# Performance work log

Measured on AMD Instinct MI355X. Metric: run time of the kernel, lower is better.

The kernel has to match this reference:

```python
import jax, jax.numpy as jnp
import numpy as np

N, NV, E0, HID, L, H = 32768, 64, 524288, 128, 4, 8
D = HID // H  # 16
SCALE = 1.0 / float(np.sqrt(D))


def _segment_softmax(logits, seg, num_segments):
    # numerically stable softmax grouped by destination node (leading axis = edges)
    m = jax.ops.segment_max(logits, seg, num_segments=num_segments)
    m = jnp.where(jnp.isfinite(m), m, 0.0)  # guard empty segments
    e = jnp.exp(logits - m[seg])
    s = jax.ops.segment_sum(e, seg, num_segments=num_segments)
    return e / (s[seg] + 1e-16)


def _forward(ei0, ei1, x_op, x_v, Wk, bk, Wq, bq, Wv, bv, Wa, ba, skip,
             a_rel, m_rel, p_rel, jk_w_in, jk_b_in, jk_w_out, jk_b_out,
             nm_w0, nm_b0, nm_w1, nm_b1, nm_w2, nm_b2, nm_w3, nm_b3,
             nm_w4, nm_b4, nm_w5, nm_b5, nm_w6, nm_b6,
             gm_w0, gm_b0, gm_w1, gm_b1):
    s0, d0 = ei0[0], ei0[1]
    s1, d1 = ei1[0], ei1[1]
    nm_ws = (nm_w0, nm_w1, nm_w2, nm_w3, nm_w4, nm_w5, nm_w6)
    nm_bs = (nm_b0, nm_b1, nm_b2, nm_b3, nm_b4, nm_b5, nm_b6)
    proj = lambda x, W, b: (x @ W.T + b).reshape(x.shape[0], H, D)
    outs_v = []
    for l in range(L):  # HGTConv layers (node types: 0='op', 1='virtual_op')
        k_op = proj(x_op, Wk[l, 0], bk[l, 0])
        q_op = proj(x_op, Wq[l, 0], bq[l, 0])
        v_op = proj(x_op, Wv[l, 0], bv[l, 0])
        q_v = proj(x_v, Wq[l, 1], bq[l, 1])  # virtual nodes only receive messages
        # relation 0: op -> op
        k0 = jnp.einsum('nhd,hde->nhe', k_op, a_rel[l, 0])
        v0 = jnp.einsum('nhd,hde->nhe', v_op, m_rel[l, 0])
        lg0 = jnp.sum(q_op[d0] * k0[s0], -1) * p_rel[l, 0] * SCALE  # [E0, H]
        al0 = _segment_softmax(lg0, d0, N)
        agg_op = jax.ops.segment_sum(al0[..., None] * v0[s0], d0, num_segments=N).reshape(N, HID)
        # relation 1: op -> virtual_op
        k1 = jnp.einsum('nhd,hde->nhe', k_op, a_rel[l, 1])
        v1 = jnp.einsum('nhd,hde->nhe', v_op, m_rel[l, 1])
        lg1 = jnp.sum(q_v[d1] * k1[s1], -1) * p_rel[l, 1] * SCALE  # [E1, H]
        al1 = _segment_softmax(lg1, d1, NV)
        agg_v = jax.ops.segment_sum(al1[..., None] * v1[s1], d1, num_segments=NV).reshape(NV, HID)
        # target-specific output projection + sigmoid-gated skip (in == out channels)
        o_op = jax.nn.gelu(agg_op, approximate=False) @ Wa[l, 0].T + ba[l, 0]
        g = jax.nn.sigmoid(skip[l, 0])
        x_op = g * o_op + (1.0 - g) * x_op
        o_v = jax.nn.gelu(agg_v, approximate=False) @ Wa[l, 1].T + ba[l, 1]
        g = jax.nn.sigmoid(skip[l, 1])
        x_v = g * o_v + (1.0 - g) * x_v
        outs_v.append(x_v)
    # JK via MultiheadAttention: seq = L layers, batch = NV virtual nodes
    xs = jnp.stack(outs_v)  # [L, NV, HID]
    qkv = xs @ jk_w_in.T + jk_b_in
    q, k, v = jnp.split(qkv, 3, axis=-1)
    q = q.reshape(L, NV, H, D)
    k = k.reshape(L, NV, H, D)
    v = v.reshape(L, NV, H, D)
    attn = jax.nn.softmax(jnp.einsum('qbhd,kbhd->bhqk', q, k) * SCALE, axis=-1)
    o = jnp.einsum('bhqk,kbhd->qbhd', attn, v).reshape(L, NV, HID)
    o = o @ jk_w_out.T + jk_b_out
    h = o.sum(0)  # [NV, HID]; batch_size == NV (1 virtual node per graph)
    for w_, b_ in zip(nm_ws[:-1], nm_bs[:-1]):  # node MLP (GELU hidden layers)
        h = jax.nn.gelu(h @ w_.T + b_, approximate=False)
    h = h @ nm_ws[-1].T + nm_bs[-1]  # [NV, 1]
    h = jax.nn.gelu(h @ gm_w0.T + gm_b0, approximate=False)  # graph MLP
    h = h @ gm_w1.T + gm_b1  # [NV, 1]
    return h[:, 0]  # squeeze(1)


def setup_inputs() -> dict:
    key = jax.random.key(0)
    ks = iter(jax.random.split(key, 64))
    nk = lambda: next(ks)
    w = lambda shape, s: jax.random.normal(nk(), shape, jnp.float32) * s
    inp = {}
    inp['x_op'] = jax.random.normal(nk(), (N, HID), jnp.float32)
    inp['x_v'] = jax.random.normal(nk(), (NV, HID), jnp.float32)
    src0 = jax.random.randint(nk(), (E0,), 0, N, jnp.int32)
    dst0 = jax.random.randint(nk(), (E0,), 0, N, jnp.int32)
    inp['ei0'] = jnp.stack([src0, dst0])
    batch_op = jax.random.randint(nk(), (N,), 0, NV, jnp.int32)  # graph id of each op node
    inp['ei1'] = jnp.stack([jnp.arange(N, dtype=jnp.int32), batch_op])
    for nm in ('Wk', 'Wq', 'Wv', 'Wa'):
        inp[nm] = w((L, 2, HID, HID), 0.1)
    for nm in ('bk', 'bq', 'bv', 'ba'):
        inp[nm] = jnp.zeros((L, 2, HID), jnp.float32)
    inp['skip'] = jnp.ones((L, 2), jnp.float32)
    inp['a_rel'] = w((L, 2, H, D, D), 0.25)
    inp['m_rel'] = w((L, 2, H, D, D), 0.25)
    inp['p_rel'] = jnp.ones((L, 2, H), jnp.float32)
    inp['jk_w_in'] = w((3 * HID, HID), 0.1)
    inp['jk_b_in'] = jnp.zeros((3 * HID,), jnp.float32)
    inp['jk_w_out'] = w((HID, HID), 0.1)
    inp['jk_b_out'] = jnp.zeros((HID,), jnp.float32)
    dims = [128, 64, 32, 16, 8, 4, 2, 1]  # _get_mlp_layer_dims(128, 1) + final out
    for i in range(7):
        inp[f'nm_w{i}'] = w((dims[i + 1], dims[i]), (2.0 / dims[i]) ** 0.5)
        inp[f'nm_b{i}'] = jnp.zeros((dims[i + 1],), jnp.float32)
    inp['gm_w0'] = w((2, 1), 1.0)
    inp['gm_b0'] = jnp.zeros((2,), jnp.float32)
    inp['gm_w1'] = w((1, 2), 0.7)
    inp['gm_b1'] = jnp.zeros((1,), jnp.float32)
    return inp


def reference(x_op, x_v, ei0, ei1, Wk, bk, Wq, bq, Wv, bv, Wa, ba, skip,
              a_rel, m_rel, p_rel, jk_w_in, jk_b_in, jk_w_out, jk_b_out,
              nm_w0, nm_b0, nm_w1, nm_b1, nm_w2, nm_b2, nm_w3, nm_b3,
              nm_w4, nm_b4, nm_w5, nm_b5, nm_w6, nm_b6,
              gm_w0, gm_b0, gm_w1, gm_b1):
    return _forward(ei0, ei1, x_op, x_v, Wk, bk, Wq, bq, Wv, bv, Wa, ba, skip,
                    a_rel, m_rel, p_rel, jk_w_in, jk_b_in, jk_w_out, jk_b_out,
                    nm_w0, nm_b0, nm_w1, nm_b1, nm_w2, nm_b2, nm_w3, nm_b3,
                    nm_w4, nm_b4, nm_w5, nm_b5, nm_w6, nm_b6,
                    gm_w0, gm_b0, gm_w1, gm_b1)
```

## Files before the change

kernel.cpp:

```cpp
#include <hip/hip_runtime.h>

#define NN   32768
#define NV   64
#define E0E  524288
#define HID  128
#define NL   4
#define NH   8
#define DH   16
#define SCALE 0.25f
#define LDA  136
#define CAP0 64
#define CAP1 1024

typedef __attribute__((ext_vector_type(8))) short short8;
typedef __attribute__((ext_vector_type(4))) float f32x4;

__device__ __forceinline__ float gelu_f(float x) {
  return 0.5f * x * (1.0f + erff(x * 0.7071067811865475f));
}
__device__ __forceinline__ float sigmoid_f(float x) {
  return 1.0f / (1.0f + __expf(-x));
}
__device__ __forceinline__ unsigned short f2bf(float x) {
  unsigned u = __float_as_uint(x);
  return (unsigned short)((u + 0x7FFFu + ((u >> 16) & 1u)) >> 16);
}
__device__ __forceinline__ float bf2f(unsigned short h) {
  return __uint_as_float(((unsigned)h) << 16);
}
__device__ __forceinline__ unsigned short f2h(float x) {
  union { _Float16 h; unsigned short u; } cv;
  cv.h = (_Float16)x;
  return cv.u;
}
__device__ __forceinline__ float h2f(unsigned short u) {
  union { _Float16 h; unsigned short u; } cv;
  cv.u = u;
  return (float)cv.h;
}
__device__ __forceinline__ float f16lo(unsigned u) { return h2f((unsigned short)(u & 0xffffu)); }
__device__ __forceinline__ float f16hi(unsigned u) { return h2f((unsigned short)(u >> 16)); }

union SMu {
  struct { unsigned short Ah[64][LDA]; unsigned short Al[64][LDA]; } a;
  struct { float xr[HID]; float xn[HID]; } v;
};

__device__ __forceinline__ void stage_A(unsigned short Ah[][LDA], unsigned short Al[][LDA],
                                        int t, const float* __restrict__ A, int m0, int gelu) {
  #pragma unroll
  for (int i = 0; i < 8; ++i) {
    int idx = t + 256 * i;
    int m = idx >> 5, c4 = (idx & 31) * 4;
    float4 v = *(const float4*)(A + (size_t)(m0 + m) * HID + c4);
    if (gelu) { v.x = gelu_f(v.x); v.y = gelu_f(v.y); v.z = gelu_f(v.z); v.w = gelu_f(v.w); }
    unsigned short h0 = f2bf(v.x), h1 = f2bf(v.y), h2 = f2bf(v.z), h3 = f2bf(v.w);
    *(ushort4*)&Ah[m][c4] = make_ushort4(h0, h1, h2, h3);
    *(ushort4*)&Al[m][c4] = make_ushort4(f2bf(v.x - bf2f(h0)), f2bf(v.y - bf2f(h1)),
                                         f2bf(v.z - bf2f(h2)), f2bf(v.w - bf2f(h3)));
  }
}

__device__ __forceinline__ void mfma_pass(const unsigned short Ah[][LDA],
    const unsigned short Al[][LDA], int t, const unsigned short* __restrict__ Wf,
    f32x4 acc[2][4]) {
  const int w = t >> 6, lane = t & 63, c16 = lane & 15, quad = lane >> 4;
  #pragma unroll
  for (int ks = 0; ks < 4; ++ks) {
    short8 ah[4], al[4];
    #pragma unroll
    for (int s = 0; s < 4; ++s) {
      ah[s] = *(const short8*)&Ah[16 * s + c16][ks * 32 + quad * 8];
      al[s] = *(const short8*)&Al[16 * s + c16][ks * 32 + quad * 8];
    }
    #pragma unroll
    for (int j = 0; j < 2; ++j) {
      const unsigned short* bp = Wf + (size_t)(((2 * w + j) * 4 + ks) * 64 + lane) * 8;
      short8 bh = *(const short8*)bp;
      short8 bl = *(const short8*)(bp + 16384);
      #pragma unroll
      for (int s = 0; s < 4; ++s) {
        acc[j][s] = __builtin_amdgcn_mfma_f32_16x16x32_bf16(ah[s], bh, acc[j][s], 0, 0, 0);
        acc[j][s] = __builtin_amdgcn_mfma_f32_16x16x32_bf16(ah[s], bl, acc[j][s], 0, 0, 0);
        acc[j][s] = __builtin_amdgcn_mfma_f32_16x16x32_bf16(al[s], bh, acc[j][s], 0, 0, 0);
      }
    }
  }
}

__device__ __forceinline__ void proj_q(const unsigned short Ah[][LDA],
    const unsigned short Al[][LDA], int t, int m0,
    const unsigned short* __restrict__ WqF, const float* __restrict__ bq0,
    float* __restrict__ Pq) {
  const int w = t >> 6, c16 = t & 15, quad = (t & 63) >> 4;
  f32x4 acc[2][4] = {};
  mfma_pass(Ah, Al, t, WqF, acc);
  #pragma unroll
  for (int j = 0; j < 2; ++j) {
    const int col = (2 * w + j) * 16 + c16;
    const float bb = bq0[col];
    #pragma unroll
    for (int s = 0; s < 4; ++s)
      #pragma unroll
      for (int r = 0; r < 4; ++r) {
        int m = m0 + 16 * s + quad * 4 + r;
        Pq[(size_t)m * HID + col] = acc[j][s][r] + bb;
      }
  }
}

__device__ __forceinline__ void proj_kv(const unsigned short Ah[][LDA],
    const unsigned short Al[][LDA], int t, int m0,
    const unsigned short* __restrict__ WfK, const float* __restrict__ bK,
    const float* __restrict__ bV, unsigned int* __restrict__ dst) {
  const int w = t >> 6, c16 = t & 15, quad = (t & 63) >> 4;
  unsigned kp[2][4][2];
  {
    f32x4 accK[2][4] = {};
    mfma_pass(Ah, Al, t, WfK, accK);
    #pragma unroll
    for (int j = 0; j < 2; ++j) {
      const float bbk = bK[(2 * w + j) * 16 + c16];
      #pragma unroll
      for (int s = 0; s < 4; ++s)
        #pragma unroll
        for (int rr = 0; rr < 2; ++rr)
          kp[j][s][rr] = (unsigned)f2h(accK[j][s][2 * rr] + bbk)
                       | ((unsigned)f2h(accK[j][s][2 * rr + 1] + bbk) << 16);
    }
  }
  f32x4 accV[2][4] = {};
  mfma_pass(Ah, Al, t, WfK + 32768, accV);
  #pragma unroll
  for (int j = 0; j < 2; ++j) {
    const int col = (2 * w + j) * 16 + c16;
    const float bbv = bV[col];
    #pragma unroll
    for (int s = 0; s < 4; ++s)
      #pragma unroll
      for (int r = 0; r < 4; ++r) {
        int m = m0 + 16 * s + quad * 4 + r;
        unsigned pk = (kp[j][s][r >> 1] >> ((r & 1) * 16)) & 0xffffu;
        unsigned pv = (unsigned)f2h(accV[j][s][r] + bbv);
        dst[(size_t)m * HID + col] = pk | (pv << 16);
      }
  }
}

__global__ __launch_bounds__(256) void k_setup(
    const float* __restrict__ Wk, const float* __restrict__ Wv,
    const float* __restrict__ bk, const float* __restrict__ bv,
    const float* __restrict__ a_rel, const float* __restrict__ m_rel,
    const float* __restrict__ p_rel,
    float* __restrict__ CW, float* __restrict__ CB) {
  int blk = blockIdx.x, t = threadIdx.x;
  int l = blk >> 2, mat = blk & 3;
  int rel = mat >> 1;
  int isK = ((mat & 1) == 0);
  const float* W  = (isK ? Wk : Wv) + (size_t)(l * 2) * HID * HID;
  const float* bb = (isK ? bk : bv) + (l * 2) * HID;
  const float* R  = (isK ? a_rel : m_rel) + (size_t)((l * 2 + rel) * NH) * DH * DH;
  float* cw = CW + (size_t)blk * HID * HID;
  float* cb = CB + blk * HID;
  for (int o = t; o < HID * HID; o += 256) {
    int j = o >> 7, c = o & 127;
    int h = j >> 4, e = j & 15;
    float sc = isK ? (p_rel[(l * 2 + rel) * NH + h] * SCALE) : 1.0f;
    float s = 0.f;
    #pragma unroll
    for (int d = 0; d < DH; ++d)
      s += W[(size_t)(h * DH + d) * HID + c] * R[h * 256 + d * 16 + e];
    cw[(size_t)j * HID + c] = s * sc;
  }
  if (t < HID) {
    int j = t, h = j >> 4, e = j & 15;
    float sc = isK ? (p_rel[(l * 2 + rel) * NH + h] * SCALE) : 1.0f;
    float s = 0.f;
    #pragma unroll
    for (int d = 0; d < DH; ++d) s += bb[h * DH + d] * R[h * 256 + d * 16 + e];
    cb[j] = s * sc;
  }
}

__global__ __launch_bounds__(256) void k_frag(const float* __restrict__ CW,
                                              const float* __restrict__ Wq,
                                              const float* __restrict__ Wa,
                                              unsigned short* __restrict__ FW) {
  int m = blockIdx.x, t = threadIdx.x;
  const float* src = (m < 16) ? (CW + (size_t)m * HID * HID)
                   : (m < 20) ? (Wq + (size_t)((m - 16) * 2) * HID * HID)
                              : (Wa + (size_t)((m - 20) * 2) * HID * HID);
  unsigned short* hi = FW + (size_t)m * 32768;
  unsigned short* lo = hi + 16384;
  for (int idx = t; idx < 16384; idx += 256) {
    int j = idx & 7, lane = (idx >> 3) & 63, ks = (idx >> 9) & 3, nt = idx >> 11;
    int n = nt * 16 + (lane & 15);
    int k = ks * 32 + (lane >> 4) * 8 + j;
    float x = src[(size_t)n * HID + k];
    unsigned short h = f2bf(x);
    hi[idx] = h;
    lo[idx] = f2bf(x - bf2f(h));
  }
}

struct PreArgs {
  const int *src0, *dst0, *src1, *dst1;
  int *cnt0, *cnt1, *colB0, *colB1;
  const float* x_op; const unsigned short* FW; const float *bq, *CB;
  float* Pq; unsigned int *Pkv0, *Pkv1;
  const float *x_v, *Wq1, *bq1; float* qv;
};

__launch_bounds__(256)
__global__ void k_pre(PreArgs a) {
  __shared__ SMu sm;
  int bx = blockIdx.x, t = threadIdx.x;
  if (bx < E0E / 1024) {
    int base = bx * 1024 + t;
    #pragma unroll
    for (int i = 0; i < 4; ++i) {
      int e = base + i * 256;
      int d = a.dst0[e];
      int pos = atomicAdd(&a.cnt0[d], 1);
      if (pos < CAP0) a.colB0[((size_t)d << 6) + pos] = a.src0[e];
    }
    return;
  }
  bx -= E0E / 1024;
  if (bx < NN / 1024) {
    int base = bx * 1024 + t;
    #pragma unroll
    for (int i = 0; i < 4; ++i) {
      int e = base + i * 256;
      int d = a.dst1[e];
      int pos = atomicAdd(&a.cnt1[d], 1);
      if (pos < CAP1) a.colB1[((size_t)d << 10) + pos] = a.src1[e];
    }
    return;
  }
  bx -= NN / 1024;
  if (bx < 3 * (NN / 64)) {
    int y = bx >> 9, tile = bx & 511;
    int m0 = tile * 64;
    stage_A(sm.a.Ah, sm.a.Al, t, a.x_op, m0, 0);
    __syncthreads();
    if (y == 0)      proj_q (sm.a.Ah, sm.a.Al, t, m0, a.FW + (size_t)16 * 32768, a.bq, a.Pq);
    else if (y == 1) proj_kv(sm.a.Ah, sm.a.Al, t, m0, a.FW, a.CB, a.CB + HID, a.Pkv0);
    else             proj_kv(sm.a.Ah, sm.a.Al, t, m0, a.FW + (size_t)2 * 32768,
                             a.CB + 2 * HID, a.CB + 3 * HID, a.Pkv1);
    return;
  }
  bx -= 3 * (NN / 64);
  if (t < HID) sm.v.xr[t] = a.x_v[bx * HID + t];
  __syncthreads();
  if (t < HID) {
    float s = a.bq1[t];
    const float4* wr = (const float4*)(a.Wq1 + (size_t)t * HID);
    const float4* xx = (const float4*)sm.v.xr;
    #pragma unroll 8
    for (int c = 0; c < HID / 4; ++c) {
      float4 w4 = wr[c], x4 = xx[c];
      s += x4.x * w4.x + x4.y * w4.y + x4.z * w4.z + x4.w * w4.w;
    }
    a.qv[bx * HID + t] = s;
  }
}

__launch_bounds__(256)
__global__ void k_edges(const float* __restrict__ Pq, const unsigned int* __restrict__ Pkv0,
                        const unsigned int* __restrict__ Pkv1,
                        const int* __restrict__ cnt0, const int* __restrict__ colB0,
                        float* __restrict__ agg, const float* __restrict__ qv,
                        const int* __restrict__ cnt1, const int* __restrict__ colB1,
                        float* __restrict__ part, int e0blocks) {
  int lane = threadIdx.x & 63;
  if (blockIdx.x < e0blocks) {
    int n = blockIdx.x * 4 + (threadIdx.x >> 6);
    float2 q = *(const float2*)(Pq + (size_t)n * HID + 2 * lane);
    int cnt = cnt0[n]; if (cnt > CAP0) cnt = CAP0;
    int e = n << 6, e1 = (n << 6) + cnt;
    float acc0 = 0.f, acc1 = 0.f, wsum = 0.f;
    for (; e + 8 <= e1; e += 8) {
      const uint2* r[8];
      #pragma unroll
      for (int u = 0; u < 8; ++u)
        r[u] = (const uint2*)(Pkv0 + ((size_t)colB0[e + u] << 7) + 2 * lane);
      uint2 kv[8];
      #pragma unroll
      for (int u = 0; u < 8; ++u) kv[u] = *r[u];
      float p[8];
      #pragma unroll
      for (int u = 0; u < 8; ++u)
        p[u] = q.x * f16lo(kv[u].x) + q.y * f16lo(kv[u].y);
      #pragma unroll
      for (int u = 0; u < 8; ++u) {
        p[u] += __shfl_xor(p[u], 1); p[u] += __shfl_xor(p[u], 2); p[u] += __shfl_xor(p[u], 4);
      }
      #pragma unroll
      for (int u = 0; u < 8; ++u) {
        float wg = __expf(p[u]);
        wsum += wg; acc0 += wg * f16hi(kv[u].x); acc1 += wg * f16hi(kv[u].y);
      }
    }
    for (; e < e1; ++e) {
      uint2 kv = *(const uint2*)(Pkv0 + ((size_t)colB0[e] << 7) + 2 * lane);
      float p = q.x * f16lo(kv.x) + q.y * f16lo(kv.y);
      p += __shfl_xor(p, 1); p += __shfl_xor(p, 2); p += __shfl_xor(p, 4);
      float wg = __expf(p);
      wsum += wg; acc0 += wg * f16hi(kv.x); acc1 += wg * f16hi(kv.y);
    }
    float inv = 1.0f / (wsum + 1e-16f);
    *(float2*)(agg + (size_t)n * HID + 2 * lane) = make_float2(acc0 * inv, acc1 * inv);
  } else {
    int b2 = blockIdx.x - e0blocks;
    int g = b2 >> 3, ch = b2 & 7;
    int w = threadIdx.x >> 6;
    int slot = ch * 4 + w;
    float2 q = *(const float2*)(qv + g * HID + 2 * lane);
    int tot = cnt1[g]; if (tot > CAP1) tot = CAP1;
    int base = g << 10;
    int len = (tot + 31) >> 5;
    int s0 = base + slot * len;
    int s1 = s0 + len; int lim = base + tot; if (s1 > lim) s1 = lim;
    float acc0 = 0.f, acc1 = 0.f, wsum = 0.f;
    int e = s0;
    for (; e + 4 <= s1; e += 4) {
      uint2 ka = *(const uint2*)(Pkv1 + ((size_t)colB1[e]     << 7) + 2 * lane);
      uint2 kb = *(const uint2*)(Pkv1 + ((size_t)colB1[e + 1] << 7) + 2 * lane);
      uint2 kc = *(const uint2*)(Pkv1 + ((size_t)colB1[e + 2] << 7) + 2 * lane);
      uint2 kd = *(const uint2*)(Pkv1 + ((size_t)colB1[e + 3] << 7) + 2 * lane);
      float pa = q.x * f16lo(ka.x) + q.y * f16lo(ka.y);
      float pb = q.x * f16lo(kb.x) + q.y * f16lo(kb.y);
      float pc = q.x * f16lo(kc.x) + q.y * f16lo(kc.y);
      float pd = q.x * f16lo(kd.x) + q.y * f16lo(kd.y);
      pa += __shfl_xor(pa, 1); pb += __shfl_xor(pb, 1); pc += __shfl_xor(pc, 1); pd += __shfl_xor(pd, 1);
      pa += __shfl_xor(pa, 2); pb += __shfl_xor(pb, 2); pc += __shfl_xor(pc, 2); pd += __shfl_xor(pd, 2);
      pa += __shfl_xor(pa, 4); pb += __shfl_xor(pb, 4); pc += __shfl_xor(pc, 4); pd += __shfl_xor(pd, 4);
      float wa = __expf(pa), wb = __expf(pb), wc = __expf(pc), wd = __expf(pd);
      wsum += (wa + wb) + (wc + wd);
      acc0 += wa * f16hi(ka.x) + wb * f16hi(kb.x) + wc * f16hi(kc.x) + wd * f16hi(kd.x);
      acc1 += wa * f16hi(ka.y) + wb * f16hi(kb.y) + wc * f16hi(kc.y) + wd * f16hi(kd.y);
    }
    for (; e < s1; ++e) {
      uint2 kv = *(const uint2*)(Pkv1 + ((size_t)colB1[e] << 7) + 2 * lane);
      float p = q.x * f16lo(kv.x) + q.y * f16lo(kv.y);
      p += __shfl_xor(p, 1); p += __shfl_xor(p, 2); p += __shfl_xor(p, 4);
      float ww = __expf(p);
      wsum += ww; acc0 += ww * f16hi(kv.x); acc1 += ww * f16hi(kv.y);
    }
    float* pp = part + (size_t)(g * 32 + slot) * 192;
    pp[lane] = acc0; pp[64 + lane] = acc1; pp[128 + lane] = wsum;
  }
}

struct PArgs {
  const float *agg; const unsigned short *WaF_l; const float *ba_l0, *skip_l0, *xold;
  float *xop;
  const float *part, *Wa_l1, *ba_l1, *skip_l1, *xvold;
  float *xv, *outsv_l, *qv;
  const float *Wq_n1, *bq_n1;
  int do_qv;
  const unsigned short *WqF_n, *CWF_n;
  const float *bq_n0, *CB_n;
  float *Pq; unsigned int *Pkv0, *Pkv1;
  int mode;
};

__device__ __forceinline__ void vtail(SMu& sm, int t, int v, const PArgs& f) {
  if (t < 64) {
    float a0 = 0.f, a1 = 0.f, ws2 = 0.f;
    for (int s = 0; s < 32; ++s) {
      const float* p = f.part + (size_t)(v * 32 + s) * 192;
      a0 += p[t]; a1 += p[64 + t]; ws2 += p[128 + t];
    }
    float inv = 1.0f / (ws2 + 1e-16f);
    sm.v.xr[2 * t]     = gelu_f(a0 * inv);
    sm.v.xr[2 * t + 1] = gelu_f(a1 * inv);
  }
  __syncthreads();
  if (t < HID) {
    float s = f.ba_l1[t];
    const float4* wr = (const float4*)(f.Wa_l1 + (size_t)t * HID);
    const float4* xx = (const float4*)sm.v.xr;
    #pragma unroll 8
    for (int c = 0; c < HID / 4; ++c) {
      float4 w4 = wr[c], x4 = xx[c];
      s += x4.x * w4.x + x4.y * w4.y + x4.z * w4.z + x4.w * w4.w;
    }
    float gg = sigmoid_f(*f.skip_l1);
    float nv2 = gg * s + (1.f - gg) * f.xvold[v * HID + t];
    f.xv[v * HID + t] = nv2;
    f.outsv_l[v * HID + t] = nv2;
    sm.v.xn[t] = nv2;
  }
  __syncthreads();
  if (f.do_qv && t < HID) {
    float s = f.bq_n1[t];
    const float4* wr = (const float4*)(f.Wq_n1 + (size_t)t * HID);
    const float4* xx = (const float4*)sm.v.xn;
    #pragma unroll 8
    for (int c = 0; c < HID / 4; ++c) {
      float4 w4 = wr[c], x4 = xx[c];
      s += x4.x * w4.x + x4.y * w4.y + x4.z * w4.z + x4.w * w4.w;
    }
    f.qv[v * HID + t] = s;
  }
}

__launch_bounds__(256)
__global__ void k_post(PArgs f) {
  __shared__ SMu sm;
  const int t = threadIdx.x;
  int bx = blockIdx.x;
  if (f.mode == 2) { vtail(sm, t, bx, f); return; }
  if (bx >= NN / 64) { vtail(sm, t, bx - NN / 64, f); return; }
  const int m0 = bx * 64;
  stage_A(sm.a.Ah, sm.a.Al, t, f.agg, m0, 1);
  __syncthreads();
  f32x4 acc[2][4] = {};
  mfma_pass(sm.a.Ah, sm.a.Al, t, f.WaF_l, acc);
  const int w = t >> 6, c16 = t & 15, quad = (t & 63) >> 4;
  float g = sigmoid_f(*f.skip_l0), gm1 = 1.0f - g;
  #pragma unroll
  for (int j = 0; j < 2; ++j) {
    const int col = (2 * w + j) * 16 + c16;
    const float bb = f.ba_l0[col];
    #pragma unroll
    for (int s = 0; s < 4; ++s)
      #pragma unroll
      for (int r = 0; r < 4; ++r) {
        int lm = 16 * s + quad * 4 + r;
        float v = acc[j][s][r] + bb;
        v = g * v + gm1 * f.xold[(size_t)(m0 + lm) * HID + col];
        acc[j][s][r] = v;
        if (f.mode == 0)
          f.xop[(size_t)(m0 + lm) * HID + col] = v;
      }
  }
  __syncthreads();
  #pragma unroll
  for (int j = 0; j < 2; ++j) {
    const int col = (2 * w + j) * 16 + c16;
    #pragma unroll
    for (int s = 0; s < 4; ++s)
      #pragma unroll
      for (int r = 0; r < 4; ++r) {
        int lm = 16 * s + quad * 4 + r;
        float v = acc[j][s][r];
        unsigned short h = f2bf(v);
        sm.a.Ah[lm][col] = h;
        sm.a.Al[lm][col] = f2bf(v - bf2f(h));
      }
  }
  __syncthreads();
  if (f.mode == 1) {
    proj_kv(sm.a.Ah, sm.a.Al, t, m0, f.CWF_n + (size_t)2 * 32768,
            f.CB_n + 2 * HID, f.CB_n + 3 * HID, f.Pkv1);
    return;
  }
  proj_q (sm.a.Ah, sm.a.Al, t, m0, f.WqF_n, f.bq_n0, f.Pq);
  proj_kv(sm.a.Ah, sm.a.Al, t, m0, f.CWF_n, f.CB_n, f.CB_n + HID, f.Pkv0);
  proj_kv(sm.a.Ah, sm.a.Al, t, m0, f.CWF_n + (size_t)2 * 32768,
          f.CB_n + 2 * HID, f.CB_n + 3 * HID, f.Pkv1);
}

struct TailW {
  const float *win, *bin, *wout, *bout;
  const float *nw0, *nb0, *nw1, *nb1, *nw2, *nb2, *nw3, *nb3, *nw4, *nb4, *nw5, *nb5, *nw6, *nb6;
  const float *gw0, *gb0, *gw1, *gb1;
};

__launch_bounds__(128)
__global__ void k_final(const float* __restrict__ outsv, TailW tw, float* __restrict__ outp) {
  __shared__ float xs[4][HID], qq[4][HID], kk[4][HID], vv[4][HID], oo[4][HID];
  __shared__ float att[NH][4][4];
  __shared__ float hb[HID], tb[64];
  int b = blockIdx.x, t = threadIdx.x;
  for (int l = 0; l < 4; ++l) xs[l][t] = outsv[(size_t)(l * NV + b) * HID + t];
  __syncthreads();
  for (int l = 0; l < 4; ++l) {
    float sq = tw.bin[t], sk = tw.bin[t + 128], sv = tw.bin[t + 256];
    const float* wq = tw.win + (size_t)t * HID;
    const float* wk = tw.win + (size_t)(t + 128) * HID;
    const float* wv = tw.win + (size_t)(t + 256) * HID;
    for (int c = 0; c < HID; ++c) {
      float x = xs[l][c];
      sq += x * wq[c]; sk += x * wk[c]; sv += x * wv[c];
    }
    qq[l][t] = sq; kk[l][t] = sk; vv[l][t] = sv;
  }
  __syncthreads();
  {
    int h = t >> 4, ql = (t >> 2) & 3, kl = t & 3;
    float s = 0.f;
    #pragma unroll
    for (int d = 0; d < DH; ++d) s += qq[ql][h * DH + d] * kk[kl][h * DH + d];
    att[h][ql][kl] = s * SCALE;
  }
  __syncthreads();
  if (t < 32) {
    int h = t >> 2, ql = t & 3;
    float m = att[h][ql][0];
    for (int k2 = 1; k2 < 4; ++k2) m = fmaxf(m, att[h][ql][k2]);
    float e[4], s = 0.f;
    for (int k2 = 0; k2 < 4; ++k2) { e[k2] = __expf(att[h][ql][k2] - m); s += e[k2]; }
    for (int k2 = 0; k2 < 4; ++k2) att[h][ql][k2] = e[k2] / s;
  }
  __syncthreads();
  {
    int h = t >> 4;
    #pragma unroll
    for (int ql = 0; ql < 4; ++ql) {
      float s = 0.f;
      #pragma unroll
      for (int kl = 0; kl < 4; ++kl) s += att[h][ql][kl] * vv[kl][t];
      oo[ql][t] = s;
    }
  }
  __syncthreads();
  {
    float s = 0.f;
    const float* wr = tw.wout + (size_t)t * HID;
    for (int l = 0; l < 4; ++l) {
      float ss = tw.bout[t];
      for (int c = 0; c < HID; ++c) ss += oo[l][c] * wr[c];
      s += ss;
    }
    hb[t] = s;
  }
  __syncthreads();
  if (t < 64) { float s = tw.nb0[t]; const float* wr = tw.nw0 + t * 128; for (int c = 0; c < 128; ++c) s += hb[c] * wr[c]; tb[t] = gelu_f(s); }
  __syncthreads();
  if (t < 32) { float s = tw.nb1[t]; const float* wr = tw.nw1 + t * 64;  for (int c = 0; c < 64;  ++c) s += tb[c] * wr[c]; hb[t] = gelu_f(s); }
  __syncthreads();
  if (t < 16) { float s = tw.nb2[t]; const float* wr = tw.nw2 + t * 32;  for (int c = 0; c < 32;  ++c) s += hb[c] * wr[c]; tb[t] = gelu_f(s); }
  __syncthreads();
  if (t < 8)  { float s = tw.nb3[t]; const float* wr = tw.nw3 + t * 16;  for (int c = 0; c < 16;  ++c) s += tb[c] * wr[c]; hb[t] = gelu_f(s); }
  __syncthreads();
  if (t < 4)  { float s = tw.nb4[t]; const float* wr = tw.nw4 + t * 8;   for (int c = 0; c < 8;   ++c) s += hb[c] * wr[c]; tb[t] = gelu_f(s); }
  __syncthreads();
  if (t < 2)  { float s = tw.nb5[t]; const float* wr = tw.nw5 + t * 4;   for (int c = 0; c < 4;   ++c) s += tb[c] * wr[c]; hb[t] = gelu_f(s); }
  __syncthreads();
  if (t == 0) {
    float s = hb[0] * tw.nw6[0] + hb[1] * tw.nw6[1] + tw.nb6[0];
    float g0 = gelu_f(s * tw.gw0[0] + tw.gb0[0]);
    float g1 = gelu_f(s * tw.gw0[1] + tw.gb0[1]);
    outp[b] = g0 * tw.gw1[0] + g1 * tw.gw1[1] + tw.gb1[0];
  }
}

extern "C" void kernel_launch(void* const* d_in, const int* in_sizes, int n_in,
                              void* d_out, int out_size, void* d_ws, size_t ws_size,
                              hipStream_t stream) {
  const float* x_op = (const float*)d_in[0];
  const float* x_v  = (const float*)d_in[1];
  const int*   ei0  = (const int*)d_in[2];
  const int*   ei1  = (const int*)d_in[3];
  const float* Wk   = (const float*)d_in[4];
  const float* Wq   = (const float*)d_in[5];
  const float* Wv   = (const float*)d_in[6];
  const float* Wa   = (const float*)d_in[7];
  const float* bk   = (const float*)d_in[8];
  const float* bq   = (const float*)d_in[9];
  const float* bv   = (const float*)d_in[10];
  const float* ba   = (const float*)d_in[11];
  const float* skip = (const float*)d_in[12];
  const float* a_rel = (const float*)d_in[13];
  const float* m_rel = (const float*)d_in[14];
  const float* p_rel = (const float*)d_in[15];
  (void)in_sizes; (void)n_in; (void)out_size; (void)ws_size;

  char* wsp = (char*)d_ws;
  size_t off = 0;
  auto alloc = [&](size_t bytes) -> void* {
    void* p = wsp + off;
    off += (bytes + 255) & ~(size_t)255;
    return p;
  };
  float* Pq    = (float*)alloc((size_t)NN * HID * 4);
  unsigned int* Pkv0 = (unsigned int*)alloc((size_t)NN * HID * 4);
  unsigned int* Pkv1 = (unsigned int*)alloc((size_t)NN * HID * 4);
  float* xop   = (float*)alloc((size_t)NN * HID * 4);
  float* agg   = (float*)alloc((size_t)NN * HID * 4);
  float* CW    = (float*)alloc((size_t)16 * HID * HID * 4);
  float* CB    = (float*)alloc((size_t)16 * HID * 4);
  unsigned short* FW = (unsigned short*)alloc((size_t)24 * 32768 * 2);
  float* xv    = (float*)alloc((size_t)NV * HID * 4);
  float* qv    = (float*)alloc((size_t)NV * HID * 4);
  float* outsv = (float*)alloc((size_t)NL * NV * HID * 4);
  float* part  = (float*)alloc((size_t)NV * 32 * 192 * 4);
  int* cnt0    = (int*)alloc((size_t)NN * 4);
  int* colB0   = (int*)alloc((size_t)NN * CAP0 * 4);
  int* cnt1    = (int*)alloc((size_t)NV * 4);
  int* colB1   = (int*)alloc((size_t)NV * CAP1 * 4);

  hipMemsetAsync(cnt0, 0, (size_t)NN * 4, stream);
  hipMemsetAsync(cnt1, 0, (size_t)NV * 4, stream);

  k_setup<<<16, 256, 0, stream>>>(Wk, Wv, bk, bv, a_rel, m_rel, p_rel, CW, CB);
  k_frag<<<24, 256, 0, stream>>>(CW, Wq, Wa, FW);

  PreArgs pa;
  pa.src0 = ei0; pa.dst0 = ei0 + E0E;
  pa.src1 = ei1; pa.dst1 = ei1 + NN;
  pa.cnt0 = cnt0; pa.cnt1 = cnt1; pa.colB0 = colB0; pa.colB1 = colB1;
  pa.x_op = x_op; pa.FW = FW; pa.bq = bq; pa.CB = CB;
  pa.Pq = Pq; pa.Pkv0 = Pkv0; pa.Pkv1 = Pkv1;
  pa.x_v = x_v; pa.Wq1 = Wq + (size_t)1 * HID * HID; pa.bq1 = bq + HID; pa.qv = qv;
  k_pre<<<E0E / 1024 + NN / 1024 + 3 * (NN / 64) + NV, 256, 0, stream>>>(pa);

  for (int l = 0; l < NL; ++l) {
    int e0b = (l < NL - 1) ? NN / 4 : 0;
    k_edges<<<e0b + NV * 8, 256, 0, stream>>>(Pq, Pkv0, Pkv1, cnt0, colB0, agg,
                                              qv, cnt1, colB1, part, e0b);
    PArgs f;
    f.agg = agg;
    f.WaF_l = FW + (size_t)(20 + l) * 32768;
    f.ba_l0 = ba + (l * 2 + 0) * HID;
    f.skip_l0 = skip + l * 2 + 0;
    f.xold = (l == 0) ? x_op : xop;
    f.xop = xop;
    f.part = part;
    f.Wa_l1 = Wa + (size_t)(l * 2 + 1) * HID * HID;
    f.ba_l1 = ba + (l * 2 + 1) * HID;
    f.skip_l1 = skip + l * 2 + 1;
    f.xvold = (l == 0) ? x_v : xv;
    f.xv = xv;
    f.outsv_l = outsv + (size_t)l * NV * HID;
    f.qv = qv;
    int ln = (l + 1) & 3;
    f.Wq_n1 = Wq + (size_t)(ln * 2 + 1) * HID * HID;
    f.bq_n1 = bq + (ln * 2 + 1) * HID;
    f.do_qv = (l < NL - 1) ? 1 : 0;
    f.WqF_n = FW + (size_t)(16 + ln) * 32768;
    f.CWF_n = FW + (size_t)(ln * 4) * 32768;
    f.bq_n0 = bq + (ln * 2 + 0) * HID;
    f.CB_n  = CB + ln * 4 * HID;
    f.Pq = Pq; f.Pkv0 = Pkv0; f.Pkv1 = Pkv1;
    f.mode = (l < 2) ? 0 : (l == 2) ? 1 : 2;
    k_post<<<(l < NL - 1) ? (NN / 64 + NV) : NV, 256, 0, stream>>>(f);
  }

  TailW tw;
  tw.win  = (const float*)d_in[16]; tw.bin  = (const float*)d_in[17];
  tw.wout = (const float*)d_in[18]; tw.bout = (const float*)d_in[19];
  tw.nw0 = (const float*)d_in[20]; tw.nb0 = (const float*)d_in[21];
  tw.nw1 = (const float*)d_in[22]; tw.nb1 = (const float*)d_in[23];
  tw.nw2 = (const float*)d_in[24]; tw.nb2 = (const float*)d_in[25];
  tw.nw3 = (const float*)d_in[26]; tw.nb3 = (const float*)d_in[27];
  tw.nw4 = (const float*)d_in[28]; tw.nb4 = (const float*)d_in[29];
  tw.nw5 = (const float*)d_in[30]; tw.nb5 = (const float*)d_in[31];
  tw.nw6 = (const float*)d_in[32]; tw.nb6 = (const float*)d_in[33];
  tw.gw0 = (const float*)d_in[34]; tw.gb0 = (const float*)d_in[35];
  tw.gw1 = (const float*)d_in[36]; tw.gb1 = (const float*)d_in[37];
  k_final<<<NV, 128, 0, stream>>>(outsv, tw, (float*)d_out);
}
```

Measured before the change: 628.3 us.

## Split post kernel into skip-update and parallel projection kernels; fuse weight setup

The per-layer post kernel used to run the output projection, the skip update and all three next-layer projections in one block per 64-row tile. It now writes the updated features to ping-pong buffers and launches a second kernel with one block per (tile, projection). That triples the block count for the projection stage, at the cost of an extra launch and re-reading the features from global memory. It also merges the weight setup and fragment-packing kernels through shared memory, and doubles the edge work per block in the CSR-build phase.

```diff
diff --git a/kernel.cpp b/kernel.cpp
--- a/kernel.cpp
+++ b/kernel.cpp
@@ -147,51 +147,56 @@
   }
 }
 
-__global__ __launch_bounds__(256) void k_setup(
+__global__ __launch_bounds__(256) void k_sf(
     const float* __restrict__ Wk, const float* __restrict__ Wv,
     const float* __restrict__ bk, const float* __restrict__ bv,
     const float* __restrict__ a_rel, const float* __restrict__ m_rel,
-    const float* __restrict__ p_rel,
-    float* __restrict__ CW, float* __restrict__ CB) {
-  int blk = blockIdx.x, t = threadIdx.x;
-  int l = blk >> 2, mat = blk & 3;
-  int rel = mat >> 1;
-  int isK = ((mat & 1) == 0);
-  const float* W  = (isK ? Wk : Wv) + (size_t)(l * 2) * HID * HID;
-  const float* bb = (isK ? bk : bv) + (l * 2) * HID;
-  const float* R  = (isK ? a_rel : m_rel) + (size_t)((l * 2 + rel) * NH) * DH * DH;
-  float* cw = CW + (size_t)blk * HID * HID;
-  float* cb = CB + blk * HID;
-  for (int o = t; o < HID * HID; o += 256) {
-    int j = o >> 7, c = o & 127;
-    int h = j >> 4, e = j & 15;
-    float sc = isK ? (p_rel[(l * 2 + rel) * NH + h] * SCALE) : 1.0f;
-    float s = 0.f;
-    #pragma unroll
-    for (int d = 0; d < DH; ++d)
-      s += W[(size_t)(h * DH + d) * HID + c] * R[h * 256 + d * 16 + e];
-    cw[(size_t)j * HID + c] = s * sc;
-  }
-  if (t < HID) {
-    int j = t, h = j >> 4, e = j & 15;
-    float sc = isK ? (p_rel[(l * 2 + rel) * NH + h] * SCALE) : 1.0f;
-    float s = 0.f;
-    #pragma unroll
-    for (int d = 0; d < DH; ++d) s += bb[h * DH + d] * R[h * 256 + d * 16 + e];
-    cb[j] = s * sc;
-  }
-}
-
-__global__ __launch_bounds__(256) void k_frag(const float* __restrict__ CW,
-                                              const float* __restrict__ Wq,
-                                              const float* __restrict__ Wa,
-                                              unsigned short* __restrict__ FW) {
+    const float* __restrict__ p_rel, const float* __restrict__ Wq,
+    const float* __restrict__ Wa, float* __restrict__ CB,
+    unsigned short* __restrict__ FW) {
+  __shared__ float cwl[HID * HID];
   int m = blockIdx.x, t = threadIdx.x;
-  const float* src = (m < 16) ? (CW + (size_t)m * HID * HID)
-                   : (m < 20) ? (Wq + (size_t)((m - 16) * 2) * HID * HID)
-                              : (Wa + (size_t)((m - 20) * 2) * HID * HID);
   unsigned short* hi = FW + (size_t)m * 32768;
   unsigned short* lo = hi + 16384;
+  if (m < 16) {
+    int l = m >> 2, mat = m & 3;
+    int rel = mat >> 1;
+    int isK = ((mat & 1) == 0);
+    const float* W  = (isK ? Wk : Wv) + (size_t)(l * 2) * HID * HID;
+    const float* bb = (isK ? bk : bv) + (l * 2) * HID;
+    const float* R  = (isK ? a_rel : m_rel) + (size_t)((l * 2 + rel) * NH) * DH * DH;
+    for (int o = t; o < HID * HID; o += 256) {
+      int j = o >> 7, c = o & 127;
+      int h = j >> 4, e = j & 15;
+      float sc = isK ? (p_rel[(l * 2 + rel) * NH + h] * SCALE) : 1.0f;
+      float s = 0.f;
+      #pragma unroll
+      for (int d = 0; d < DH; ++d)
+        s += W[(size_t)(h * DH + d) * HID + c] * R[h * 256 + d * 16 + e];
+      cwl[j * HID + c] = s * sc;
+    }
+    if (t < HID) {
+      int j = t, h = j >> 4, e = j & 15;
+      float sc = isK ? (p_rel[(l * 2 + rel) * NH + h] * SCALE) : 1.0f;
+      float s = 0.f;
+      #pragma unroll
+      for (int d = 0; d < DH; ++d) s += bb[h * DH + d] * R[h * 256 + d * 16 + e];
+      CB[m * HID + j] = s * sc;
+    }
+    __syncthreads();
+    for (int idx = t; idx < 16384; idx += 256) {
+      int j = idx & 7, lane = (idx >> 3) & 63, ks = (idx >> 9) & 3, nt = idx >> 11;
+      int n = nt * 16 + (lane & 15);
+      int k = ks * 32 + (lane >> 4) * 8 + j;
+      float x = cwl[n * HID + k];
+      unsigned short h = f2bf(x);
+      hi[idx] = h;
+      lo[idx] = f2bf(x - bf2f(h));
+    }
+    return;
+  }
+  const float* src = (m < 20) ? (Wq + (size_t)((m - 16) * 2) * HID * HID)
+                              : (Wa + (size_t)((m - 20) * 2) * HID * HID);
   for (int idx = t; idx < 16384; idx += 256) {
     int j = idx & 7, lane = (idx >> 3) & 63, ks = (idx >> 9) & 3, nt = idx >> 11;
     int n = nt * 16 + (lane & 15);
@@ -215,10 +220,10 @@
 __global__ void k_pre(PreArgs a) {
   __shared__ SMu sm;
   int bx = blockIdx.x, t = threadIdx.x;
-  if (bx < E0E / 1024) {
-    int base = bx * 1024 + t;
-    #pragma unroll
-    for (int i = 0; i < 4; ++i) {
+  if (bx < E0E / 2048) {
+    int base = bx * 2048 + t;
+    #pragma unroll
+    for (int i = 0; i < 8; ++i) {
       int e = base + i * 256;
       int d = a.dst0[e];
       int pos = atomicAdd(&a.cnt0[d], 1);
@@ -226,11 +231,11 @@
     }
     return;
   }
-  bx -= E0E / 1024;
-  if (bx < NN / 1024) {
-    int base = bx * 1024 + t;
-    #pragma unroll
-    for (int i = 0; i < 4; ++i) {
+  bx -= E0E / 2048;
+  if (bx < NN / 2048) {
+    int base = bx * 2048 + t;
+    #pragma unroll
+    for (int i = 0; i < 8; ++i) {
       int e = base + i * 256;
       int d = a.dst1[e];
       int pos = atomicAdd(&a.cnt1[d], 1);
@@ -238,7 +243,7 @@
     }
     return;
   }
-  bx -= NN / 1024;
+  bx -= NN / 2048;
   if (bx < 3 * (NN / 64)) {
     int y = bx >> 9, tile = bx & 511;
     int m0 = tile * 64;
@@ -355,15 +360,11 @@
 
 struct PArgs {
   const float *agg; const unsigned short *WaF_l; const float *ba_l0, *skip_l0, *xold;
-  float *xop;
+  float *xcur;
   const float *part, *Wa_l1, *ba_l1, *skip_l1, *xvold;
   float *xv, *outsv_l, *qv;
   const float *Wq_n1, *bq_n1;
-  int do_qv;
-  const unsigned short *WqF_n, *CWF_n;
-  const float *bq_n0, *CB_n;
-  float *Pq; unsigned int *Pkv0, *Pkv1;
-  int mode;
+  int do_qv, vonly;
 };
 
 __device__ __forceinline__ void vtail(SMu& sm, int t, int v, const PArgs& f) {
@@ -408,11 +409,11 @@
 }
 
 __launch_bounds__(256)
-__global__ void k_post(PArgs f) {
+__global__ void k_post_a(PArgs f) {
   __shared__ SMu sm;
   const int t = threadIdx.x;
   int bx = blockIdx.x;
-  if (f.mode == 2) { vtail(sm, t, bx, f); return; }
+  if (f.vonly) { vtail(sm, t, bx, f); return; }
   if (bx >= NN / 64) { vtail(sm, t, bx - NN / 64, f); return; }
   const int m0 = bx * 64;
   stage_A(sm.a.Ah, sm.a.Al, t, f.agg, m0, 1);
@@ -431,37 +432,28 @@
       for (int r = 0; r < 4; ++r) {
         int lm = 16 * s + quad * 4 + r;
         float v = acc[j][s][r] + bb;
-        v = g * v + gm1 * f.xold[(size_t)(m0 + lm) * HID + col];
-        acc[j][s][r] = v;
-        if (f.mode == 0)
-          f.xop[(size_t)(m0 + lm) * HID + col] = v;
+        f.xcur[(size_t)(m0 + lm) * HID + col] =
+            g * v + gm1 * f.xold[(size_t)(m0 + lm) * HID + col];
       }
   }
-  __syncthreads();
-  #pragma unroll
-  for (int j = 0; j < 2; ++j) {
-    const int col = (2 * w + j) * 16 + c16;
-    #pragma unroll
-    for (int s = 0; s < 4; ++s)
-      #pragma unroll
-      for (int r = 0; r < 4; ++r) {
-        int lm = 16 * s + quad * 4 + r;
-        float v = acc[j][s][r];
-        unsigned short h = f2bf(v);
-        sm.a.Ah[lm][col] = h;
-        sm.a.Al[lm][col] = f2bf(v - bf2f(h));
-      }
-  }
-  __syncthreads();
-  if (f.mode == 1) {
-    proj_kv(sm.a.Ah, sm.a.Al, t, m0, f.CWF_n + (size_t)2 * 32768,
-            f.CB_n + 2 * HID, f.CB_n + 3 * HID, f.Pkv1);
-    return;
-  }
-  proj_q (sm.a.Ah, sm.a.Al, t, m0, f.WqF_n, f.bq_n0, f.Pq);
-  proj_kv(sm.a.Ah, sm.a.Al, t, m0, f.CWF_n, f.CB_n, f.CB_n + HID, f.Pkv0);
-  proj_kv(sm.a.Ah, sm.a.Al, t, m0, f.CWF_n + (size_t)2 * 32768,
-          f.CB_n + 2 * HID, f.CB_n + 3 * HID, f.Pkv1);
+}
+
+__launch_bounds__(256)
+__global__ void k_post_b(const float* __restrict__ X, const unsigned short* __restrict__ WqF,
+                         const unsigned short* __restrict__ CWF,
+                         const float* __restrict__ bq0, const float* __restrict__ CBl,
+                         float* __restrict__ Pq, unsigned int* __restrict__ Pkv0,
+                         unsigned int* __restrict__ Pkv1, int y_base) {
+  __shared__ SMu sm;
+  const int t = threadIdx.x;
+  int y = y_base + (blockIdx.x >> 9), tile = blockIdx.x & 511;
+  int m0 = tile * 64;
+  stage_A(sm.a.Ah, sm.a.Al, t, X, m0, 0);
+  __syncthreads();
+  if (y == 0)      proj_q (sm.a.Ah, sm.a.Al, t, m0, WqF, bq0, Pq);
+  else if (y == 1) proj_kv(sm.a.Ah, sm.a.Al, t, m0, CWF, CBl, CBl + HID, Pkv0);
+  else             proj_kv(sm.a.Ah, sm.a.Al, t, m0, CWF + (size_t)2 * 32768,
+                           CBl + 2 * HID, CBl + 3 * HID, Pkv1);
 }
 
 struct TailW {
@@ -580,9 +572,9 @@
   float* Pq    = (float*)alloc((size_t)NN * HID * 4);
   unsigned int* Pkv0 = (unsigned int*)alloc((size_t)NN * HID * 4);
   unsigned int* Pkv1 = (unsigned int*)alloc((size_t)NN * HID * 4);
-  float* xop   = (float*)alloc((size_t)NN * HID * 4);
+  float* xopA  = (float*)alloc((size_t)NN * HID * 4);
+  float* xopB  = (float*)alloc((size_t)NN * HID * 4);
   float* agg   = (float*)alloc((size_t)NN * HID * 4);
-  float* CW    = (float*)alloc((size_t)16 * HID * HID * 4);
   float* CB    = (float*)alloc((size_t)16 * HID * 4);
   unsigned short* FW = (unsigned short*)alloc((size_t)24 * 32768 * 2);
   float* xv    = (float*)alloc((size_t)NV * HID * 4);
@@ -597,8 +589,7 @@
   hipMemsetAsync(cnt0, 0, (size_t)NN * 4, stream);
   hipMemsetAsync(cnt1, 0, (size_t)NV * 4, stream);
 
-  k_setup<<<16, 256, 0, stream>>>(Wk, Wv, bk, bv, a_rel, m_rel, p_rel, CW, CB);
-  k_frag<<<24, 256, 0, stream>>>(CW, Wq, Wa, FW);
+  k_sf<<<24, 256, 0, stream>>>(Wk, Wv, bk, bv, a_rel, m_rel, p_rel, Wq, Wa, CB, FW);
 
   PreArgs pa;
   pa.src0 = ei0; pa.dst0 = ei0 + E0E;
@@ -607,19 +598,21 @@
   pa.x_op = x_op; pa.FW = FW; pa.bq = bq; pa.CB = CB;
   pa.Pq = Pq; pa.Pkv0 = Pkv0; pa.Pkv1 = Pkv1;
   pa.x_v = x_v; pa.Wq1 = Wq + (size_t)1 * HID * HID; pa.bq1 = bq + HID; pa.qv = qv;
-  k_pre<<<E0E / 1024 + NN / 1024 + 3 * (NN / 64) + NV, 256, 0, stream>>>(pa);
+  k_pre<<<E0E / 2048 + NN / 2048 + 3 * (NN / 64) + NV, 256, 0, stream>>>(pa);
 
   for (int l = 0; l < NL; ++l) {
     int e0b = (l < NL - 1) ? NN / 4 : 0;
     k_edges<<<e0b + NV * 8, 256, 0, stream>>>(Pq, Pkv0, Pkv1, cnt0, colB0, agg,
                                               qv, cnt1, colB1, part, e0b);
+    float* xold = (l == 0) ? (float*)x_op : ((l & 1) ? xopA : xopB);
+    float* xcur = (l & 1) ? xopB : xopA;
     PArgs f;
     f.agg = agg;
     f.WaF_l = FW + (size_t)(20 + l) * 32768;
     f.ba_l0 = ba + (l * 2 + 0) * HID;
     f.skip_l0 = skip + l * 2 + 0;
-    f.xold = (l == 0) ? x_op : xop;
-    f.xop = xop;
+    f.xold = xold;
+    f.xcur = xcur;
     f.part = part;
     f.Wa_l1 = Wa + (size_t)(l * 2 + 1) * HID * HID;
     f.ba_l1 = ba + (l * 2 + 1) * HID;
@@ -632,13 +625,15 @@
     f.Wq_n1 = Wq + (size_t)(ln * 2 + 1) * HID * HID;
     f.bq_n1 = bq + (ln * 2 + 1) * HID;
     f.do_qv = (l < NL - 1) ? 1 : 0;
-    f.WqF_n = FW + (size_t)(16 + ln) * 32768;
-    f.CWF_n = FW + (size_t)(ln * 4) * 32768;
-    f.bq_n0 = bq + (ln * 2 + 0) * HID;
-    f.CB_n  = CB + ln * 4 * HID;
-    f.Pq = Pq; f.Pkv0 = Pkv0; f.Pkv1 = Pkv1;
-    f.mode = (l < 2) ? 0 : (l == 2) ? 1 : 2;
-    k_post<<<(l < NL - 1) ? (NN / 64 + NV) : NV, 256, 0, stream>>>(f);
+    f.vonly = (l == NL - 1) ? 1 : 0;
+    k_post_a<<<(l < NL - 1) ? (NN / 64 + NV) : NV, 256, 0, stream>>>(f);
+    if (l < NL - 1) {
+      int nsl = (l < 2) ? 3 : 1;
+      int yb  = (l < 2) ? 0 : 2;
+      k_post_b<<<nsl * (NN / 64), 256, 0, stream>>>(
+          xcur, FW + (size_t)(16 + ln) * 32768, FW + (size_t)(ln * 4) * 32768,
+          bq + (size_t)ln * 2 * HID, CB + (size_t)ln * 4 * HID, Pq, Pkv0, Pkv1, yb);
+    }
   }
 
   TailW tw;
```

Result: faster. 560.6 us (-10.8%).
